# Performance work log

Hardware: AMD Instinct MI355X
Metric: run time of the kernel (lower is better)

Reference implementation:

```python
import jax, jax.numpy as jnp
import numpy as np

IN_F = 4096
OUT_F = 4096
GROUPSIZE = 128
NUM_GROUPS = IN_F // GROUPSIZE  # 32


def setup_inputs() -> dict:
    key = jax.random.key(0)
    k1, k2, k3, k4 = jax.random.split(key, 4)
    x = jax.random.normal(k1, (4, 2048, IN_F), dtype=jnp.float32)
    imin = jnp.iinfo(jnp.int32).min
    imax = jnp.iinfo(jnp.int32).max
    qweight = jax.random.randint(k2, (IN_F // 8, OUT_F), imin, imax, dtype=jnp.int32)
    qzeros = jax.random.randint(k3, (NUM_GROUPS, OUT_F // 8), imin, imax, dtype=jnp.int32)
    scales = jax.random.uniform(k4, (NUM_GROUPS, OUT_F), dtype=jnp.float32,
                                minval=1e-3, maxval=2e-2)
    return {"x": x, "qweight": qweight, "qzeros": qzeros, "scales": scales}


def _unpack_rows(q):
    # q: int32 [in/8, out] -> float nibbles [in, out]; nibble i of a word is bits 4i..4i+3
    u = q.astype(jnp.uint32)
    shifts = (4 * jnp.arange(8, dtype=jnp.uint32))[None, :, None]  # [1,8,1]
    nib = (u[:, None, :] >> shifts) & jnp.uint32(0xF)              # [in/8, 8, out]
    return nib.reshape(q.shape[0] * 8, q.shape[1]).astype(jnp.float32)


def _unpack_cols(q):
    # q: int32 [g, out/8] -> float nibbles [g, out]
    u = q.astype(jnp.uint32)
    shifts = (4 * jnp.arange(8, dtype=jnp.uint32))[None, None, :]  # [1,1,8]
    nib = (u[:, :, None] >> shifts) & jnp.uint32(0xF)              # [g, out/8, 8]
    return nib.reshape(q.shape[0], q.shape[1] * 8).astype(jnp.float32)


def _dequant(qweight, qzeros, scales):
    # GPTQ dequant: w = scale[g] * (q - (z[g] + 1))
    q = _unpack_rows(qweight)                      # [IN_F, OUT_F]
    z = _unpack_cols(qzeros) + 1.0                 # [G, OUT_F]
    qg = q.reshape(NUM_GROUPS, GROUPSIZE, OUT_F)
    w = (qg - z[:, None, :]) * scales[:, None, :]
    return w.reshape(IN_F, OUT_F)


def reference(x, qweight, qzeros, scales):
    w = _dequant(qweight, qzeros, scales)          # [IN_F, OUT_F]
    # x: [B, S, IN_F] @ w -> [B, S, OUT_F]
    return jnp.einsum('bsi,io->bso', x, w)
```

## Files before the change

kernel.cpp:

```cpp
#include <hip/hip_runtime.h>
#include <stdint.h>

#define IN_F   4096
#define OUT_F  4096
#define M_ROWS 8192
#define KT     (IN_F / 64)

typedef __attribute__((ext_vector_type(8))) short  bf16x8;
typedef __attribute__((ext_vector_type(4))) float  f32x4;

__device__ __forceinline__ short f2bf(float f) {
    union { float f; uint32_t u; } v; v.f = f;
    uint32_t r = v.u + 0x7FFFu + ((v.u >> 16) & 1u);
    return (short)(r >> 16);
}

__device__ __forceinline__ void load_lds16(const void* gsrc, void* lds) {
    __builtin_amdgcn_global_load_lds(
        (const __attribute__((address_space(1))) uint32_t*)gsrc,
        (__attribute__((address_space(3))) uint32_t*)lds,
        16, 0, 0);
}

__global__ void dequant_wt_kernel(const int* __restrict__ qweight,
                                  const int* __restrict__ qzeros,
                                  const float* __restrict__ scales,
                                  short* __restrict__ wt)
{
    int t  = blockIdx.x * blockDim.x + threadIdx.x;
    int n  = t >> 9;
    int kw = t & 511;
    int g  = kw >> 4;

    float s = scales[g * OUT_F + n];
    uint32_t zw = (uint32_t)qzeros[g * (OUT_F / 8) + (n >> 3)];
    float z1 = (float)((zw >> (4 * (n & 7))) & 0xFu) + 1.0f;
    uint32_t q = (uint32_t)qweight[kw * OUT_F + n];

    bf16x8 out;
#pragma unroll
    for (int i = 0; i < 8; ++i) {
        float w = s * ((float)((q >> (4 * i)) & 0xFu) - z1);
        out[i] = f2bf(w);
    }
    *reinterpret_cast<bf16x8*>(&wt[(size_t)n * IN_F + kw * 8]) = out;
}

__global__ void xconv_kernel(const float* __restrict__ x, short* __restrict__ xb)
{
    int t = blockIdx.x * blockDim.x + threadIdx.x;
    const float4* src = reinterpret_cast<const float4*>(x) + (size_t)t * 2;
    float4 a = src[0], b = src[1];
    bf16x8 h;
    h[0] = f2bf(a.x); h[1] = f2bf(a.y); h[2] = f2bf(a.z); h[3] = f2bf(a.w);
    h[4] = f2bf(b.x); h[5] = f2bf(b.y); h[6] = f2bf(b.z); h[7] = f2bf(b.w);
    reinterpret_cast<bf16x8*>(xb)[t] = h;
}

#define A_SLOT 32768
#define B_SLOT 32768

__global__ __launch_bounds__(512, 1) void gemm8_kernel(
    const short* __restrict__ Xb,
    const short* __restrict__ WT,
    float* __restrict__ C)
{
    __shared__ short AsBuf[3 * 256 * 64];
    __shared__ short BsBuf[2 * 256 * 64];
    char* const Abase = (char*)AsBuf;
    char* const Bbase = (char*)BsBuf;

    const int tid  = threadIdx.x;
    const int lane = tid & 63;
    const int wid  = tid >> 6;
    const int wr   = wid >> 2;
    const int wc   = wid & 3;

    const int row0 = blockIdx.y * 256;
    const int col0 = blockIdx.x * 256;

    const int rL0 = tid >> 3;
    const int csw = ((tid & 7) << 3) ^ ((rL0 & 7) << 3);
    const short* gA[4]; const short* gB[4]; int dOff[4];
#pragma unroll
    for (int L = 0; L < 4; ++L) {
        const int r = L * 64 + rL0;
        gA[L] = Xb + (size_t)(row0 + r) * IN_F + csw;
        gB[L] = WT + (size_t)(col0 + r) * IN_F + csw;
        dOff[L] = L * 8192 + tid * 16;
    }

    const int frow = lane & 15;
    const int k0   = ((lane >> 4) << 4) ^ ((frow & 7) << 4);

    f32x4 acc[8][4] = {};

#pragma unroll
    for (int L = 0; L < 4; ++L) load_lds16(gA[L],      Abase + 0 * A_SLOT + dOff[L]);
#pragma unroll
    for (int L = 0; L < 4; ++L) load_lds16(gB[L],      Bbase + 0 * B_SLOT + dOff[L]);
#pragma unroll
    for (int L = 0; L < 4; ++L) load_lds16(gA[L] + 64, Abase + 1 * A_SLOT + dOff[L]);
    asm volatile("s_waitcnt vmcnt(4)" ::: "memory");
    __builtin_amdgcn_s_barrier();

    int sA = 0;
    int sB = 0;

    for (int t = 0; t < KT; ++t) {
        char* Ab = Abase + sA * A_SLOT;
        char* Bb = Bbase + sB * B_SLOT;
        const int sA2 = (sA >= 1) ? sA - 1 : 2;
        char* An = Abase + sA2 * A_SLOT;
        char* Bn = Bbase + (sB ^ 1) * B_SLOT;
        const bool pfB = (t + 1 < KT);
        const bool pfA = (t + 2 < KT);

#pragma unroll
        for (int ks = 0; ks < 2; ++ks) {
            const int kb = k0 ^ (ks << 6);

            bf16x8 af[8]; bf16x8 bfr[4];
#pragma unroll
            for (int m = 0; m < 8; ++m) {
                const int r = wr * 128 + m * 16 + frow;
                af[m] = *reinterpret_cast<const bf16x8*>(Ab + r * 128 + kb);
            }
#pragma unroll
            for (int n = 0; n < 4; ++n) {
                const int r = wc * 64 + n * 16 + frow;
                bfr[n] = *reinterpret_cast<const bf16x8*>(Bb + r * 128 + kb);
            }

            if (ks == 0) {
                if (pfB) {
#pragma unroll
                    for (int L = 0; L < 4; ++L)
                        load_lds16(gB[L] + (size_t)(t + 1) * 64, Bn + dOff[L]);
                }
                if (pfA) {
#pragma unroll
                    for (int L = 0; L < 4; ++L)
                        load_lds16(gA[L] + (size_t)(t + 2) * 64, An + dOff[L]);
                }
            }

            __builtin_amdgcn_s_setprio(1);
#pragma unroll
            for (int m = 0; m < 8; ++m)
#pragma unroll
                for (int n = 0; n < 4; ++n)
                    acc[m][n] = __builtin_amdgcn_mfma_f32_16x16x32_bf16(
                        af[m], bfr[n], acc[m][n], 0, 0, 0);
            __builtin_amdgcn_s_setprio(0);
        }

        if (t < KT - 2)       asm volatile("s_waitcnt vmcnt(4)" ::: "memory");
        else if (t == KT - 2) asm volatile("s_waitcnt vmcnt(0)" ::: "memory");
        __builtin_amdgcn_s_barrier();

        sA = (sA < 2) ? sA + 1 : 0;
        sB ^= 1;
    }

    const int crow = (lane >> 4) * 4;
    const int ccol = lane & 15;
#pragma unroll
    for (int fm = 0; fm < 8; ++fm)
#pragma unroll
        for (int fn = 0; fn < 4; ++fn)
#pragma unroll
            for (int r = 0; r < 4; ++r) {
                const int row = row0 + wr * 128 + fm * 16 + crow + r;
                const int col = col0 + wc * 64 + fn * 16 + ccol;
                C[(size_t)row * OUT_F + col] = acc[fm][fn][r];
            }
}

#define BM 128
#define BN 128
#define BK 64

__global__ __launch_bounds__(256, 2) void gemm_x_wt_kernel(
    const float* __restrict__ X,
    const short* __restrict__ WT,
    float* __restrict__ C)
{
    __shared__ short As2[BM * BK];
    __shared__ short Bs2[BN * BK];

    const int bn = blockIdx.x;
    const int bm = blockIdx.y;
    const int tid  = threadIdx.x;
    const int lane = tid & 63;
    const int wid  = tid >> 6;
    const int wr   = wid >> 1;
    const int wc   = wid & 1;

    const int row0 = bm * BM;
    const int col0 = bn * BN;
    const int frow = lane & 15;
    const int fk   = (lane >> 4) * 8;

    f32x4 acc[4][4] = {};

    for (int kt = 0; kt < IN_F / BK; ++kt) {
        float4 a0[4], a1[4];
#pragma unroll
        for (int j = 0; j < 4; ++j) {
            const int flat = (j * 256 + tid) * 8;
            const int r = flat >> 6;
            const int c = flat & (BK - 1);
            const float* src = X + (size_t)(row0 + r) * IN_F + kt * BK + c;
            a0[j] = *reinterpret_cast<const float4*>(src);
            a1[j] = *reinterpret_cast<const float4*>(src + 4);
        }
        __syncthreads();
#pragma unroll
        for (int j = 0; j < 4; ++j) {
            const int flat = (j * 256 + tid) * 8;
            const int r = flat >> 6;
            const int c = flat & (BK - 1);
            load_lds16(WT + (size_t)(col0 + r) * IN_F + kt * BK + c, &Bs2[flat]);
        }
#pragma unroll
        for (int j = 0; j < 4; ++j) {
            const int flat = (j * 256 + tid) * 8;
            bf16x8 h;
            h[0] = f2bf(a0[j].x); h[1] = f2bf(a0[j].y);
            h[2] = f2bf(a0[j].z); h[3] = f2bf(a0[j].w);
            h[4] = f2bf(a1[j].x); h[5] = f2bf(a1[j].y);
            h[6] = f2bf(a1[j].z); h[7] = f2bf(a1[j].w);
            *reinterpret_cast<bf16x8*>(&As2[flat]) = h;
        }
        __syncthreads();
#pragma unroll
        for (int s = 0; s < 2; ++s) {
            bf16x8 af[4], bfr[4];
#pragma unroll
            for (int m = 0; m < 4; ++m) {
                const int row = wr * 64 + m * 16 + frow;
                af[m] = *reinterpret_cast<const bf16x8*>(&As2[row * BK + s * 32 + fk]);
            }
#pragma unroll
            for (int n = 0; n < 4; ++n) {
                const int col = wc * 64 + n * 16 + frow;
                bfr[n] = *reinterpret_cast<const bf16x8*>(&Bs2[col * BK + s * 32 + fk]);
            }
#pragma unroll
            for (int m = 0; m < 4; ++m)
#pragma unroll
                for (int n = 0; n < 4; ++n)
                    acc[m][n] = __builtin_amdgcn_mfma_f32_16x16x32_bf16(
                        af[m], bfr[n], acc[m][n], 0, 0, 0);
        }
    }

    const int crow = (lane >> 4) * 4;
    const int ccol = lane & 15;
#pragma unroll
    for (int m = 0; m < 4; ++m)
#pragma unroll
        for (int n = 0; n < 4; ++n)
#pragma unroll
            for (int r = 0; r < 4; ++r) {
                const int row = row0 + wr * 64 + m * 16 + crow + r;
                const int col = col0 + wc * 64 + n * 16 + ccol;
                C[(size_t)row * OUT_F + col] = acc[m][n][r];
            }
}

extern "C" void kernel_launch(void* const* d_in, const int* in_sizes, int n_in,
                              void* d_out, int out_size, void* d_ws, size_t ws_size,
                              hipStream_t stream) {
    const float* x       = (const float*)d_in[0];
    const int*   qweight = (const int*)  d_in[1];
    const int*   qzeros  = (const int*)  d_in[2];
    const float* scales  = (const float*)d_in[3];
    float*       out     = (float*)d_out;

    const size_t WT_BYTES = (size_t)OUT_F * IN_F * 2;
    const size_t XB_BYTES = (size_t)M_ROWS * IN_F * 2;

    short* wt = (short*)d_ws;

    dequant_wt_kernel<<<(OUT_F * (IN_F / 8)) / 256, 256, 0, stream>>>(
        qweight, qzeros, scales, wt);

    if (ws_size >= WT_BYTES + XB_BYTES) {
        short* xb = (short*)((char*)d_ws + WT_BYTES);
        xconv_kernel<<<(M_ROWS * IN_F / 8) / 256, 256, 0, stream>>>(x, xb);
        dim3 grid(OUT_F / 256, M_ROWS / 256);
        gemm8_kernel<<<grid, 512, 0, stream>>>(xb, wt, out);
    } else {
        dim3 grid(OUT_F / BN, M_ROWS / BM);
        gemm_x_wt_kernel<<<grid, 256, 0, stream>>>(x, wt, out);
    }
}
```

Measured before the change: 272.5 us.

## Load B fragments directly into registers and swizzle block-to-tile mapping

The B (dequantized weight) tile no longer goes through LDS. Each wave loads its own B fragments from global memory straight into registers, double-buffered across k-steps, which frees 64KB of shared memory and removes the LDS reads for B. The grid becomes 1D, and an XCD-aware swizzle remaps block IDs to output tiles so neighbouring blocks share A and B rows in cache. The trade-off is that B is now loaded redundantly by the two wave rows, global loads are no longer coalesced through LDS, and register pressure rises with 16 extra bf16x8 registers.

```diff
diff --git a/kernel.cpp b/kernel.cpp
--- a/kernel.cpp
+++ b/kernel.cpp
@@ -58,7 +58,6 @@
 }
 
 #define A_SLOT 32768
-#define B_SLOT 32768
 
 __global__ __launch_bounds__(512, 1) void gemm8_kernel(
     const short* __restrict__ Xb,
@@ -66,9 +65,7 @@
     float* __restrict__ C)
 {
     __shared__ short AsBuf[3 * 256 * 64];
-    __shared__ short BsBuf[2 * 256 * 64];
     char* const Abase = (char*)AsBuf;
-    char* const Bbase = (char*)BsBuf;
 
     const int tid  = threadIdx.x;
     const int lane = tid & 63;
@@ -76,91 +73,92 @@
     const int wr   = wid >> 2;
     const int wc   = wid & 3;
 
-    const int row0 = blockIdx.y * 256;
-    const int col0 = blockIdx.x * 256;
+    const int bid = blockIdx.x;
+    const int swz = (bid & 7) * 64 + (bid >> 3);
+    const int row0 = (swz >> 4) * 256;
+    const int col0 = (swz & 15) * 256;
 
     const int rL0 = tid >> 3;
     const int csw = ((tid & 7) << 3) ^ ((rL0 & 7) << 3);
-    const short* gA[4]; const short* gB[4]; int dOff[4];
+    const short* gA[4]; int dOff[4];
 #pragma unroll
     for (int L = 0; L < 4; ++L) {
-        const int r = L * 64 + rL0;
-        gA[L] = Xb + (size_t)(row0 + r) * IN_F + csw;
-        gB[L] = WT + (size_t)(col0 + r) * IN_F + csw;
+        gA[L] = Xb + (size_t)(row0 + L * 64 + rL0) * IN_F + csw;
         dOff[L] = L * 8192 + tid * 16;
     }
 
     const int frow = lane & 15;
     const int k0   = ((lane >> 4) << 4) ^ ((frow & 7) << 4);
 
+    const short* gBf = WT + (size_t)(col0 + wc * 64 + frow) * IN_F + ((lane >> 4) << 3);
+
     f32x4 acc[8][4] = {};
-
-#pragma unroll
-    for (int L = 0; L < 4; ++L) load_lds16(gA[L],      Abase + 0 * A_SLOT + dOff[L]);
-#pragma unroll
-    for (int L = 0; L < 4; ++L) load_lds16(gB[L],      Bbase + 0 * B_SLOT + dOff[L]);
+    bf16x8 B0[8], B1[8];
+
+#pragma unroll
+    for (int L = 0; L < 4; ++L) load_lds16(gA[L], Abase + 0 * A_SLOT + dOff[L]);
+#pragma unroll
+    for (int n = 0; n < 4; ++n) {
+        const short* p = gBf + (size_t)n * 16 * IN_F;
+        B0[n * 2]     = *reinterpret_cast<const bf16x8*>(p);
+        B0[n * 2 + 1] = *reinterpret_cast<const bf16x8*>(p + 32);
+    }
 #pragma unroll
     for (int L = 0; L < 4; ++L) load_lds16(gA[L] + 64, Abase + 1 * A_SLOT + dOff[L]);
-    asm volatile("s_waitcnt vmcnt(4)" ::: "memory");
+    asm volatile("s_waitcnt vmcnt(12)" ::: "memory");
     __builtin_amdgcn_s_barrier();
 
-    int sA = 0;
-    int sB = 0;
-
-    for (int t = 0; t < KT; ++t) {
+    int sA  = 0;
+    int sA2 = 2;
+
+    auto body = [&](int t, bf16x8 (&Bcur)[8], bf16x8 (&Bnxt)[8]) {
         char* Ab = Abase + sA * A_SLOT;
-        char* Bb = Bbase + sB * B_SLOT;
-        const int sA2 = (sA >= 1) ? sA - 1 : 2;
-        char* An = Abase + sA2 * A_SLOT;
-        char* Bn = Bbase + (sB ^ 1) * B_SLOT;
-        const bool pfB = (t + 1 < KT);
-        const bool pfA = (t + 2 < KT);
+
+        if (t + 1 < KT) {
+#pragma unroll
+            for (int n = 0; n < 4; ++n) {
+                const short* p = gBf + (size_t)n * 16 * IN_F + (size_t)(t + 1) * 64;
+                Bnxt[n * 2]     = *reinterpret_cast<const bf16x8*>(p);
+                Bnxt[n * 2 + 1] = *reinterpret_cast<const bf16x8*>(p + 32);
+            }
+        }
+        if (t + 2 < KT) {
+            char* An = Abase + sA2 * A_SLOT;
+#pragma unroll
+            for (int L = 0; L < 4; ++L)
+                load_lds16(gA[L] + (size_t)(t + 2) * 64, An + dOff[L]);
+        }
 
 #pragma unroll
         for (int ks = 0; ks < 2; ++ks) {
             const int kb = k0 ^ (ks << 6);
-
-            bf16x8 af[8]; bf16x8 bfr[4];
+            bf16x8 af[8];
 #pragma unroll
             for (int m = 0; m < 8; ++m) {
                 const int r = wr * 128 + m * 16 + frow;
                 af[m] = *reinterpret_cast<const bf16x8*>(Ab + r * 128 + kb);
             }
-#pragma unroll
-            for (int n = 0; n < 4; ++n) {
-                const int r = wc * 64 + n * 16 + frow;
-                bfr[n] = *reinterpret_cast<const bf16x8*>(Bb + r * 128 + kb);
-            }
-
-            if (ks == 0) {
-                if (pfB) {
-#pragma unroll
-                    for (int L = 0; L < 4; ++L)
-                        load_lds16(gB[L] + (size_t)(t + 1) * 64, Bn + dOff[L]);
-                }
-                if (pfA) {
-#pragma unroll
-                    for (int L = 0; L < 4; ++L)
-                        load_lds16(gA[L] + (size_t)(t + 2) * 64, An + dOff[L]);
-                }
-            }
-
             __builtin_amdgcn_s_setprio(1);
 #pragma unroll
             for (int m = 0; m < 8; ++m)
 #pragma unroll
                 for (int n = 0; n < 4; ++n)
                     acc[m][n] = __builtin_amdgcn_mfma_f32_16x16x32_bf16(
-                        af[m], bfr[n], acc[m][n], 0, 0, 0);
+                        af[m], Bcur[n * 2 + ks], acc[m][n], 0, 0, 0);
             __builtin_amdgcn_s_setprio(0);
         }
 
-        if (t < KT - 2)       asm volatile("s_waitcnt vmcnt(4)" ::: "memory");
-        else if (t == KT - 2) asm volatile("s_waitcnt vmcnt(0)" ::: "memory");
-        __builtin_amdgcn_s_barrier();
-
-        sA = (sA < 2) ? sA + 1 : 0;
-        sB ^= 1;
+        if (t < KT - 2)       asm volatile("s_waitcnt vmcnt(12)" ::: "memory");
+        else if (t == KT - 2) asm volatile("s_waitcnt vmcnt(8)"  ::: "memory");
+        if (t < KT - 1) __builtin_amdgcn_s_barrier();
+
+        sA  = (sA  < 2) ? sA  + 1 : 0;
+        sA2 = (sA2 < 2) ? sA2 + 1 : 0;
+    };
+
+    for (int t = 0; t < KT; t += 2) {
+        body(t,     B0, B1);
+        body(t + 1, B1, B0);
     }
 
     const int crow = (lane >> 4) * 4;
@@ -290,8 +288,7 @@
     if (ws_size >= WT_BYTES + XB_BYTES) {
         short* xb = (short*)((char*)d_ws + WT_BYTES);
         xconv_kernel<<<(M_ROWS * IN_F / 8) / 256, 256, 0, stream>>>(x, xb);
-        dim3 grid(OUT_F / 256, M_ROWS / 256);
-        gemm8_kernel<<<grid, 512, 0, stream>>>(xb, wt, out);
+        gemm8_kernel<<<(M_ROWS / 256) * (OUT_F / 256), 512, 0, stream>>>(xb, wt, out);
     } else {
         dim3 grid(OUT_F / BN, M_ROWS / BM);
         gemm_x_wt_kernel<<<grid, 256, 0, stream>>>(x, wt, out);
```

After: 801.0 us. 194% more time.

## Fuse fp32-to-bf16 activation conversion into the 256x256 GEMM main loop

Applied to the files above, without the earlier changes.

Removes the separate xconv pass that wrote a bf16 copy of x to workspace. The GEMM now loads fp32 activations straight from global memory into registers, converts them to bf16 and writes them to a double-buffered LDS tile, with the conversion interleaved between MFMA phases. The three-slot A buffer becomes two slots and launch bounds now ask for 2 blocks per CU. The fallback small-tile GEMM and the workspace-size check are dropped. This saves a full write and re-read of the bf16 activation tensor, but each block now reads fp32 x (twice the bytes) with register-path loads and VALU conversion on the critical path, and register pressure from the 8x4 accumulators may limit occupancy.

```diff
diff --git a/kernel.cpp b/kernel.cpp
--- a/kernel.cpp
+++ b/kernel.cpp
@@ -46,26 +46,15 @@
     *reinterpret_cast<bf16x8*>(&wt[(size_t)n * IN_F + kw * 8]) = out;
 }
 
-__global__ void xconv_kernel(const float* __restrict__ x, short* __restrict__ xb)
-{
-    int t = blockIdx.x * blockDim.x + threadIdx.x;
-    const float4* src = reinterpret_cast<const float4*>(x) + (size_t)t * 2;
-    float4 a = src[0], b = src[1];
-    bf16x8 h;
-    h[0] = f2bf(a.x); h[1] = f2bf(a.y); h[2] = f2bf(a.z); h[3] = f2bf(a.w);
-    h[4] = f2bf(b.x); h[5] = f2bf(b.y); h[6] = f2bf(b.z); h[7] = f2bf(b.w);
-    reinterpret_cast<bf16x8*>(xb)[t] = h;
-}
-
 #define A_SLOT 32768
 #define B_SLOT 32768
 
-__global__ __launch_bounds__(512, 1) void gemm8_kernel(
-    const short* __restrict__ Xb,
+__global__ __launch_bounds__(512, 2) void gemm8_kernel(
+    const float* __restrict__ X,
     const short* __restrict__ WT,
     float* __restrict__ C)
 {
-    __shared__ short AsBuf[3 * 256 * 64];
+    __shared__ short AsBuf[2 * 256 * 64];
     __shared__ short BsBuf[2 * 256 * 64];
     char* const Abase = (char*)AsBuf;
     char* const Bbase = (char*)BsBuf;
@@ -81,12 +70,11 @@
 
     const int rL0 = tid >> 3;
     const int csw = ((tid & 7) << 3) ^ ((rL0 & 7) << 3);
-    const short* gA[4]; const short* gB[4]; int dOff[4];
+    const float* gAx[4]; const short* gB[4]; int dOff[4];
 #pragma unroll
     for (int L = 0; L < 4; ++L) {
-        const int r = L * 64 + rL0;
-        gA[L] = Xb + (size_t)(row0 + r) * IN_F + csw;
-        gB[L] = WT + (size_t)(col0 + r) * IN_F + csw;
+        gAx[L] = X  + (size_t)(row0 + L * 64 + rL0) * IN_F + csw;
+        gB[L]  = WT + (size_t)(col0 + L * 64 + rL0) * IN_F + csw;
         dOff[L] = L * 8192 + tid * 16;
     }
 
@@ -96,71 +84,155 @@
     f32x4 acc[8][4] = {};
 
 #pragma unroll
-    for (int L = 0; L < 4; ++L) load_lds16(gA[L],      Abase + 0 * A_SLOT + dOff[L]);
-#pragma unroll
-    for (int L = 0; L < 4; ++L) load_lds16(gB[L],      Bbase + 0 * B_SLOT + dOff[L]);
-#pragma unroll
-    for (int L = 0; L < 4; ++L) load_lds16(gA[L] + 64, Abase + 1 * A_SLOT + dOff[L]);
-    asm volatile("s_waitcnt vmcnt(4)" ::: "memory");
+    for (int L = 0; L < 4; ++L) load_lds16(gB[L], Bbase + 0 * B_SLOT + dOff[L]);
+#pragma unroll
+    for (int L = 0; L < 4; ++L) {
+        const float* p = gAx[L];
+        float4 a = *reinterpret_cast<const float4*>(p);
+        float4 b = *reinterpret_cast<const float4*>(p + 4);
+        bf16x8 h;
+        h[0] = f2bf(a.x); h[1] = f2bf(a.y); h[2] = f2bf(a.z); h[3] = f2bf(a.w);
+        h[4] = f2bf(b.x); h[5] = f2bf(b.y); h[6] = f2bf(b.z); h[7] = f2bf(b.w);
+        *reinterpret_cast<bf16x8*>(Abase + dOff[L]) = h;
+    }
+    asm volatile("s_waitcnt vmcnt(0) lgkmcnt(0)" ::: "memory");
     __builtin_amdgcn_s_barrier();
 
-    int sA = 0;
-    int sB = 0;
-
     for (int t = 0; t < KT; ++t) {
-        char* Ab = Abase + sA * A_SLOT;
-        char* Bb = Bbase + sB * B_SLOT;
-        const int sA2 = (sA >= 1) ? sA - 1 : 2;
-        char* An = Abase + sA2 * A_SLOT;
-        char* Bn = Bbase + (sB ^ 1) * B_SLOT;
-        const bool pfB = (t + 1 < KT);
-        const bool pfA = (t + 2 < KT);
-
-#pragma unroll
-        for (int ks = 0; ks < 2; ++ks) {
-            const int kb = k0 ^ (ks << 6);
-
-            bf16x8 af[8]; bf16x8 bfr[4];
-#pragma unroll
-            for (int m = 0; m < 8; ++m) {
-                const int r = wr * 128 + m * 16 + frow;
-                af[m] = *reinterpret_cast<const bf16x8*>(Ab + r * 128 + kb);
-            }
+        char* Ab = Abase + (t & 1) * A_SLOT;
+        char* Bb = Bbase + (t & 1) * B_SLOT;
+        char* An = Abase + ((t + 1) & 1) * A_SLOT;
+        char* Bn = Bbase + ((t + 1) & 1) * B_SLOT;
+        const bool pf = (t + 1 < KT);
+
+        if (pf) {
+#pragma unroll
+            for (int L = 0; L < 4; ++L)
+                load_lds16(gB[L] + (size_t)(t + 1) * 64, Bn + dOff[L]);
+        }
+        float4 x0a, x0b, x1a, x1b;
+        if (pf) {
+            const float* p0 = gAx[0] + (size_t)(t + 1) * 64;
+            const float* p1 = gAx[1] + (size_t)(t + 1) * 64;
+            x0a = *reinterpret_cast<const float4*>(p0);
+            x0b = *reinterpret_cast<const float4*>(p0 + 4);
+            x1a = *reinterpret_cast<const float4*>(p1);
+            x1b = *reinterpret_cast<const float4*>(p1 + 4);
+        }
+
+        {
+            const int kb = k0;
+            bf16x8 bfr[4];
 #pragma unroll
             for (int n = 0; n < 4; ++n) {
                 const int r = wc * 64 + n * 16 + frow;
                 bfr[n] = *reinterpret_cast<const bf16x8*>(Bb + r * 128 + kb);
             }
-
-            if (ks == 0) {
-                if (pfB) {
-#pragma unroll
-                    for (int L = 0; L < 4; ++L)
-                        load_lds16(gB[L] + (size_t)(t + 1) * 64, Bn + dOff[L]);
-                }
-                if (pfA) {
-#pragma unroll
-                    for (int L = 0; L < 4; ++L)
-                        load_lds16(gA[L] + (size_t)(t + 2) * 64, An + dOff[L]);
-                }
-            }
-
-            __builtin_amdgcn_s_setprio(1);
-#pragma unroll
-            for (int m = 0; m < 8; ++m)
-#pragma unroll
-                for (int n = 0; n < 4; ++n)
-                    acc[m][n] = __builtin_amdgcn_mfma_f32_16x16x32_bf16(
-                        af[m], bfr[n], acc[m][n], 0, 0, 0);
-            __builtin_amdgcn_s_setprio(0);
-        }
-
-        if (t < KT - 2)       asm volatile("s_waitcnt vmcnt(4)" ::: "memory");
-        else if (t == KT - 2) asm volatile("s_waitcnt vmcnt(0)" ::: "memory");
+            {
+                bf16x8 af[4];
+#pragma unroll
+                for (int m = 0; m < 4; ++m) {
+                    const int r = wr * 128 + m * 16 + frow;
+                    af[m] = *reinterpret_cast<const bf16x8*>(Ab + r * 128 + kb);
+                }
+                __builtin_amdgcn_s_setprio(1);
+#pragma unroll
+                for (int m = 0; m < 4; ++m)
+#pragma unroll
+                    for (int n = 0; n < 4; ++n)
+                        acc[m][n] = __builtin_amdgcn_mfma_f32_16x16x32_bf16(
+                            af[m], bfr[n], acc[m][n], 0, 0, 0);
+                __builtin_amdgcn_s_setprio(0);
+            }
+            {
+                bf16x8 ag[4];
+#pragma unroll
+                for (int m = 0; m < 4; ++m) {
+                    const int r = wr * 128 + (m + 4) * 16 + frow;
+                    ag[m] = *reinterpret_cast<const bf16x8*>(Ab + r * 128 + kb);
+                }
+                __builtin_amdgcn_s_setprio(1);
+#pragma unroll
+                for (int m = 0; m < 4; ++m)
+#pragma unroll
+                    for (int n = 0; n < 4; ++n)
+                        acc[m + 4][n] = __builtin_amdgcn_mfma_f32_16x16x32_bf16(
+                            ag[m], bfr[n], acc[m + 4][n], 0, 0, 0);
+                __builtin_amdgcn_s_setprio(0);
+            }
+        }
+
+        float4 x2a, x2b, x3a, x3b;
+        if (pf) {
+            bf16x8 h0, h1;
+            h0[0] = f2bf(x0a.x); h0[1] = f2bf(x0a.y); h0[2] = f2bf(x0a.z); h0[3] = f2bf(x0a.w);
+            h0[4] = f2bf(x0b.x); h0[5] = f2bf(x0b.y); h0[6] = f2bf(x0b.z); h0[7] = f2bf(x0b.w);
+            h1[0] = f2bf(x1a.x); h1[1] = f2bf(x1a.y); h1[2] = f2bf(x1a.z); h1[3] = f2bf(x1a.w);
+            h1[4] = f2bf(x1b.x); h1[5] = f2bf(x1b.y); h1[6] = f2bf(x1b.z); h1[7] = f2bf(x1b.w);
+            *reinterpret_cast<bf16x8*>(An + dOff[0]) = h0;
+            *reinterpret_cast<bf16x8*>(An + dOff[1]) = h1;
+            const float* p2 = gAx[2] + (size_t)(t + 1) * 64;
+            const float* p3 = gAx[3] + (size_t)(t + 1) * 64;
+            x2a = *reinterpret_cast<const float4*>(p2);
+            x2b = *reinterpret_cast<const float4*>(p2 + 4);
+            x3a = *reinterpret_cast<const float4*>(p3);
+            x3b = *reinterpret_cast<const float4*>(p3 + 4);
+        }
+
+        {
+            const int kb = k0 ^ 64;
+            bf16x8 bfr[4];
+#pragma unroll
+            for (int n = 0; n < 4; ++n) {
+                const int r = wc * 64 + n * 16 + frow;
+                bfr[n] = *reinterpret_cast<const bf16x8*>(Bb + r * 128 + kb);
+            }
+            {
+                bf16x8 af[4];
+#pragma unroll
+                for (int m = 0; m < 4; ++m) {
+                    const int r = wr * 128 + m * 16 + frow;
+                    af[m] = *reinterpret_cast<const bf16x8*>(Ab + r * 128 + kb);
+                }
+                __builtin_amdgcn_s_setprio(1);
+#pragma unroll
+                for (int m = 0; m < 4; ++m)
+#pragma unroll
+                    for (int n = 0; n < 4; ++n)
+                        acc[m][n] = __builtin_amdgcn_mfma_f32_16x16x32_bf16(
+                            af[m], bfr[n], acc[m][n], 0, 0, 0);
+                __builtin_amdgcn_s_setprio(0);
+            }
+            {
+                bf16x8 ag[4];
+#pragma unroll
+                for (int m = 0; m < 4; ++m) {
+                    const int r = wr * 128 + (m + 4) * 16 + frow;
+                    ag[m] = *reinterpret_cast<const bf16x8*>(Ab + r * 128 + kb);
+                }
+                __builtin_amdgcn_s_setprio(1);
+#pragma unroll
+                for (int m = 0; m < 4; ++m)
+#pragma unroll
+                    for (int n = 0; n < 4; ++n)
+                        acc[m + 4][n] = __builtin_amdgcn_mfma_f32_16x16x32_bf16(
+                            ag[m], bfr[n], acc[m + 4][n], 0, 0, 0);
+                __builtin_amdgcn_s_setprio(0);
+            }
+        }
+
+        if (pf) {
+            bf16x8 h2, h3;
+            h2[0] = f2bf(x2a.x); h2[1] = f2bf(x2a.y); h2[2] = f2bf(x2a.z); h2[3] = f2bf(x2a.w);
+            h2[4] = f2bf(x2b.x); h2[5] = f2bf(x2b.y); h2[6] = f2bf(x2b.z); h2[7] = f2bf(x2b.w);
+            h3[0] = f2bf(x3a.x); h3[1] = f2bf(x3a.y); h3[2] = f2bf(x3a.z); h3[3] = f2bf(x3a.w);
+            h3[4] = f2bf(x3b.x); h3[5] = f2bf(x3b.y); h3[6] = f2bf(x3b.z); h3[7] = f2bf(x3b.w);
+            *reinterpret_cast<bf16x8*>(An + dOff[2]) = h2;
+            *reinterpret_cast<bf16x8*>(An + dOff[3]) = h3;
+        }
+
+        asm volatile("s_waitcnt lgkmcnt(0)" ::: "memory");
         __builtin_amdgcn_s_barrier();
-
-        sA = (sA < 2) ? sA + 1 : 0;
-        sB ^= 1;
     }
 
     const int crow = (lane >> 4) * 4;
@@ -174,99 +246,6 @@
                 const int row = row0 + wr * 128 + fm * 16 + crow + r;
                 const int col = col0 + wc * 64 + fn * 16 + ccol;
                 C[(size_t)row * OUT_F + col] = acc[fm][fn][r];
-            }
-}
-
-#define BM 128
-#define BN 128
-#define BK 64
-
-__global__ __launch_bounds__(256, 2) void gemm_x_wt_kernel(
-    const float* __restrict__ X,
-    const short* __restrict__ WT,
-    float* __restrict__ C)
-{
-    __shared__ short As2[BM * BK];
-    __shared__ short Bs2[BN * BK];
-
-    const int bn = blockIdx.x;
-    const int bm = blockIdx.y;
-    const int tid  = threadIdx.x;
-    const int lane = tid & 63;
-    const int wid  = tid >> 6;
-    const int wr   = wid >> 1;
-    const int wc   = wid & 1;
-
-    const int row0 = bm * BM;
-    const int col0 = bn * BN;
-    const int frow = lane & 15;
-    const int fk   = (lane >> 4) * 8;
-
-    f32x4 acc[4][4] = {};
-
-    for (int kt = 0; kt < IN_F / BK; ++kt) {
-        float4 a0[4], a1[4];
-#pragma unroll
-        for (int j = 0; j < 4; ++j) {
-            const int flat = (j * 256 + tid) * 8;
-            const int r = flat >> 6;
-            const int c = flat & (BK - 1);
-            const float* src = X + (size_t)(row0 + r) * IN_F + kt * BK + c;
-            a0[j] = *reinterpret_cast<const float4*>(src);
-            a1[j] = *reinterpret_cast<const float4*>(src + 4);
-        }
-        __syncthreads();
-#pragma unroll
-        for (int j = 0; j < 4; ++j) {
-            const int flat = (j * 256 + tid) * 8;
-            const int r = flat >> 6;
-            const int c = flat & (BK - 1);
-            load_lds16(WT + (size_t)(col0 + r) * IN_F + kt * BK + c, &Bs2[flat]);
-        }
-#pragma unroll
-        for (int j = 0; j < 4; ++j) {
-            const int flat = (j * 256 + tid) * 8;
-            bf16x8 h;
-            h[0] = f2bf(a0[j].x); h[1] = f2bf(a0[j].y);
-            h[2] = f2bf(a0[j].z); h[3] = f2bf(a0[j].w);
-            h[4] = f2bf(a1[j].x); h[5] = f2bf(a1[j].y);
-            h[6] = f2bf(a1[j].z); h[7] = f2bf(a1[j].w);
-            *reinterpret_cast<bf16x8*>(&As2[flat]) = h;
-        }
-        __syncthreads();
-#pragma unroll
-        for (int s = 0; s < 2; ++s) {
-            bf16x8 af[4], bfr[4];
-#pragma unroll
-            for (int m = 0; m < 4; ++m) {
-                const int row = wr * 64 + m * 16 + frow;
-                af[m] = *reinterpret_cast<const bf16x8*>(&As2[row * BK + s * 32 + fk]);
-            }
-#pragma unroll
-            for (int n = 0; n < 4; ++n) {
-                const int col = wc * 64 + n * 16 + frow;
-                bfr[n] = *reinterpret_cast<const bf16x8*>(&Bs2[col * BK + s * 32 + fk]);
-            }
-#pragma unroll
-            for (int m = 0; m < 4; ++m)
-#pragma unroll
-                for (int n = 0; n < 4; ++n)
-                    acc[m][n] = __builtin_amdgcn_mfma_f32_16x16x32_bf16(
-                        af[m], bfr[n], acc[m][n], 0, 0, 0);
-        }
-    }
-
-    const int crow = (lane >> 4) * 4;
-    const int ccol = lane & 15;
-#pragma unroll
-    for (int m = 0; m < 4; ++m)
-#pragma unroll
-        for (int n = 0; n < 4; ++n)
-#pragma unroll
-            for (int r = 0; r < 4; ++r) {
-                const int row = row0 + wr * 64 + m * 16 + crow + r;
-                const int col = col0 + wc * 64 + n * 16 + ccol;
-                C[(size_t)row * OUT_F + col] = acc[m][n][r];
             }
 }
 
@@ -279,21 +258,11 @@
     const float* scales  = (const float*)d_in[3];
     float*       out     = (float*)d_out;
 
-    const size_t WT_BYTES = (size_t)OUT_F * IN_F * 2;
-    const size_t XB_BYTES = (size_t)M_ROWS * IN_F * 2;
-
     short* wt = (short*)d_ws;
 
     dequant_wt_kernel<<<(OUT_F * (IN_F / 8)) / 256, 256, 0, stream>>>(
         qweight, qzeros, scales, wt);
 
-    if (ws_size >= WT_BYTES + XB_BYTES) {
-        short* xb = (short*)((char*)d_ws + WT_BYTES);
-        xconv_kernel<<<(M_ROWS * IN_F / 8) / 256, 256, 0, stream>>>(x, xb);
-        dim3 grid(OUT_F / 256, M_ROWS / 256);
-        gemm8_kernel<<<grid, 512, 0, stream>>>(xb, wt, out);
-    } else {
-        dim3 grid(OUT_F / BN, M_ROWS / BM);
-        gemm_x_wt_kernel<<<grid, 256, 0, stream>>>(x, wt, out);
-    }
-}
+    dim3 grid(OUT_F / 256, M_ROWS / 256);
+    gemm8_kernel<<<grid, 512, 0, stream>>>(x, wt, out);
+}
```

Measured after the change: 381.3 us. +39.9%, slower.
